# Optimization experiments

Measured on AMD Instinct MI355X. Metric: run time of the kernel, lower is better.

## Reference

```python
import jax, jax.numpy as jnp
import numpy as np

B, S, H, N, D = 2, 2048, 1024, 16, 64  # batch, seq, hidden, heads, head_dim


def setup_inputs() -> dict:
    key = jax.random.key(0)
    ks = jax.random.split(key, 7)
    sc = 0.02
    return {
        "query": jax.random.normal(ks[0], (B, S, H), jnp.float32),
        "key": jax.random.normal(ks[1], (B, S, H), jnp.float32),
        "value": jax.random.normal(ks[2], (B, S, H), jnp.float32),
        "Wq": jax.random.normal(ks[3], (N, H, D), jnp.float32) * sc,
        "Wk": jax.random.normal(ks[4], (N, H, D), jnp.float32) * sc,
        "Wv": jax.random.normal(ks[5], (N, H, D), jnp.float32) * sc,
        "Wo": jax.random.normal(ks[6], (H, H), jnp.float32) * sc,
    }


def reference(query, key, value, Wq, Wk, Wv, Wo):
    # Per-head projections (all heads batched): q,k,v -> [B, N, S, D]
    q = jnp.einsum('bsh,nhd->bnsd', query, Wq)
    k = jnp.einsum('bsh,nhd->bnsd', key, Wk)
    v = jnp.einsum('bsh,nhd->bnsd', value, Wv)
    scale = jnp.sqrt(jnp.asarray(D, q.dtype))
    # scaled dot-product attention, no mask, dropout=0 (eval mode)
    scores = jnp.einsum('bnqd,bnkd->bnqk', q, k) / scale  # [B, N, S, S]
    attn = jax.nn.softmax(scores, axis=-1)
    ctx = jnp.einsum('bnqk,bnkd->bnqd', attn, v)  # [B, N, S, D]
    # concat heads (head order matches the module's per-head list order)
    concat = ctx.transpose(0, 2, 1, 3).reshape(B, S, N * D)  # [B, S, H]
    out = concat @ Wo  # output projection, bias-free
    return out, attn
```

## Files before the change

kernel.cpp:

```cpp
#include <hip/hip_runtime.h>
#include <hip/hip_bf16.h>

using bf16 = __hip_bfloat16;
typedef __bf16 bf16x8 __attribute__((ext_vector_type(8)));
typedef float f32x4 __attribute__((ext_vector_type(4)));

__device__ __forceinline__ void async16(const void* g, void* l) {
    __builtin_amdgcn_global_load_lds((const __attribute__((address_space(1))) void*)g,
                                     (__attribute__((address_space(3))) void*)l, 16, 0, 0);
}
__device__ __forceinline__ bf16x8 ld8(const bf16* p) {
    return *reinterpret_cast<const bf16x8*>(p);
}
__device__ __forceinline__ unsigned short bfbits(float f) {
    bf16 h = __float2bfloat16(f);
    return *reinterpret_cast<unsigned short*>(&h);
}


__global__ __launch_bounds__(256) void cast_kernel(const float* __restrict__ q, const float* __restrict__ k,
                                                   const float* __restrict__ v, bf16* __restrict__ dst) {
    int z = blockIdx.z;
    const float* src = (z == 0) ? q : (z == 1) ? k : v;
    bf16* d = dst + (size_t)z * 4194304u;
    size_t i = ((size_t)blockIdx.x * 256 + threadIdx.x) * 4;
    float4 f = *(const float4*)(src + i);
    ushort4 pk = make_ushort4(bfbits(f.x), bfbits(f.y), bfbits(f.z), bfbits(f.w));
    *(ushort4*)(d + i) = pk;
}

__global__ __launch_bounds__(256) void wt_kernel(const float* __restrict__ wq, const float* __restrict__ wk,
                                                 const float* __restrict__ wv, bf16* __restrict__ wt) {
    int z = blockIdx.z;
    const float* W = (z == 0) ? wq : (z == 1) ? wk : wv;
    bf16* Wt = wt + (size_t)z * (1024u * 1024u);
    int n = blockIdx.y, h0 = blockIdx.x * 64;
    __shared__ float tile[64][65];
    int t = threadIdx.x, row = t >> 2, cq = t & 3;
#pragma unroll
    for (int u = 0; u < 4; u++) {
        int col = cq * 16 + u * 4;
        float4 f = *(const float4*)(W + (size_t)(n * 1024 + h0 + row) * 64 + col);
        tile[row][col] = f.x; tile[row][col + 1] = f.y; tile[row][col + 2] = f.z; tile[row][col + 3] = f.w;
    }
    __syncthreads();
#pragma unroll
    for (int u = 0; u < 4; u++) {
        int hl = cq * 16 + u * 4;
        ushort4 pk = make_ushort4(bfbits(tile[hl][row]), bfbits(tile[hl + 1][row]),
                                  bfbits(tile[hl + 2][row]), bfbits(tile[hl + 3][row]));
        *(ushort4*)(Wt + (size_t)(n * 64 + row) * 1024 + h0 + hl) = pk;
    }
}

__global__ __launch_bounds__(256) void wo_kernel(const float* __restrict__ Wo, bf16* __restrict__ Wot) {
    int h0 = blockIdx.x * 64, j0 = blockIdx.y * 64;
    __shared__ float tile[64][65];
    int t = threadIdx.x, row = t >> 2, cq = t & 3;
#pragma unroll
    for (int u = 0; u < 4; u++) {
        int col = cq * 16 + u * 4;
        float4 f = *(const float4*)(Wo + (size_t)(h0 + row) * 1024 + j0 + col);
        tile[row][col] = f.x; tile[row][col + 1] = f.y; tile[row][col + 2] = f.z; tile[row][col + 3] = f.w;
    }
    __syncthreads();
#pragma unroll
    for (int u = 0; u < 4; u++) {
        int hl = cq * 16 + u * 4;
        ushort4 pk = make_ushort4(bfbits(tile[hl][row]), bfbits(tile[hl + 1][row]),
                                  bfbits(tile[hl + 2][row]), bfbits(tile[hl + 3][row]));
        *(ushort4*)(Wot + (size_t)(j0 + row) * 1024 + h0 + hl) = pk;
    }
}

__global__ __launch_bounds__(256) void proj_kernel(const bf16* __restrict__ Xall, const bf16* __restrict__ Wall,
                                                   bf16* __restrict__ qb, bf16* __restrict__ kb,
                                                   bf16* __restrict__ vt) {
    int z = blockIdx.z;
    const bf16* X = Xall + (size_t)z * (4096u * 1024u);
    const bf16* W = Wall + (size_t)z * (1024u * 1024u);
    __shared__ bf16 sA[128 * 64];
    __shared__ bf16 sB[128 * 64];
    int t = threadIdx.x, lane = t & 63, q4 = lane >> 4, cl = lane & 15, w = t >> 6;
    int wm = (w >> 1) * 64, wn = (w & 1) * 64;
    int m0 = blockIdx.x * 128, n0 = blockIdx.y * 128;
    f32x4 acc[4][4] = {};
    for (int k0 = 0; k0 < 1024; k0 += 64) {
#pragma unroll
        for (int it = 0; it < 4; it++) {
            int j = it * 256 + t;
            int row = j >> 3, sl = j & 7, g = sl ^ (row & 7);
            async16(X + (size_t)(m0 + row) * 1024 + k0 + g * 8, sA + j * 8);
            async16(W + (size_t)(n0 + row) * 1024 + k0 + g * 8, sB + j * 8);
        }
        __syncthreads();
#pragma unroll
        for (int ks = 0; ks < 2; ks++) {
            bf16x8 af[4], bfr[4];
#pragma unroll
            for (int mi = 0; mi < 4; mi++) {
                int row = wm + mi * 16 + cl;
                af[mi] = ld8(sA + row * 64 + ((ks * 4 + q4) ^ (row & 7)) * 8);
            }
#pragma unroll
            for (int ni = 0; ni < 4; ni++) {
                int row = wn + ni * 16 + cl;
                bfr[ni] = ld8(sB + row * 64 + ((ks * 4 + q4) ^ (row & 7)) * 8);
            }
#pragma unroll
            for (int mi = 0; mi < 4; mi++)
#pragma unroll
                for (int ni = 0; ni < 4; ni++)
                    acc[mi][ni] = __builtin_amdgcn_mfma_f32_16x16x32_bf16(af[mi], bfr[ni], acc[mi][ni], 0, 0, 0);
        }
        __syncthreads();
    }
    if (z < 2) {
        bf16* dst = (z == 0) ? qb : kb;
#pragma unroll
        for (int mi = 0; mi < 4; mi++)
#pragma unroll
            for (int ni = 0; ni < 4; ni++) {
                int col = n0 + wn + ni * 16 + cl;
                int hn = col >> 6, dd = col & 63;
#pragma unroll
                for (int i = 0; i < 4; i++) {
                    int row = m0 + wm + mi * 16 + q4 * 4 + i;
                    int b = row >> 11, s = row & 2047;
                    dst[(size_t)((b * 16 + hn) * 2048 + s) * 64 + dd] = __float2bfloat16(acc[mi][ni][i]);
                }
            }
    } else {
#pragma unroll
        for (int mi = 0; mi < 4; mi++)
#pragma unroll
            for (int ni = 0; ni < 4; ni++) {
                int col = n0 + wn + ni * 16 + cl;
                int hn = col >> 6, dd = col & 63;
                int row0 = m0 + wm + mi * 16 + q4 * 4;
                int b = row0 >> 11, s = row0 & 2047;
                ushort4 pk = make_ushort4(bfbits(acc[mi][ni][0]), bfbits(acc[mi][ni][1]),
                                          bfbits(acc[mi][ni][2]), bfbits(acc[mi][ni][3]));
                *(ushort4*)(vt + (size_t)((b * 16 + hn) * 64 + dd) * 2048 + s) = pk;
            }
    }
}

__global__ __launch_bounds__(256) void attn_kernel(const bf16* __restrict__ qb, const bf16* __restrict__ kb,
                                                   const bf16* __restrict__ vt, bf16* __restrict__ cc,
                                                   float* __restrict__ attn) {
    __shared__ bf16 sQ[64 * 64];
    __shared__ bf16 sK[64 * 64];
    __shared__ bf16 sV[64 * 64];
    __shared__ bf16 sP[64 * 64];
    __shared__ float srow[64];
    __shared__ float sinv[64];
    int t = threadIdx.x, lane = t & 63, q4 = lane >> 4, cl = lane & 15, w = t >> 6;
    int bn = blockIdx.y;
    int s0 = blockIdx.x * 64;
    const bf16* qh = qb + (size_t)bn * 2048 * 64;
    const bf16* kh = kb + (size_t)bn * 2048 * 64;
    const bf16* vh = vt + (size_t)bn * 64 * 2048;
    float* ah = attn + (size_t)bn * 2048 * 2048;

    if (t < 64) srow[t] = 0.f;
#pragma unroll
    for (int it = 0; it < 2; it++) {
        int j = it * 256 + t;
        int row = j >> 3, sl = j & 7, g = sl ^ (row & 7);
        async16(qh + (size_t)(s0 + row) * 64 + g * 8, sQ + j * 8);
    }

    float rs[4][4] = {};
    for (int ch = 0; ch < 32; ch++) {
#pragma unroll
        for (int it = 0; it < 2; it++) {
            int j = it * 256 + t;
            int row = j >> 3, sl = j & 7, g = sl ^ (row & 7);
            async16(kh + (size_t)(ch * 64 + row) * 64 + g * 8, sK + j * 8);
        }
        __syncthreads();
        bf16x8 bk[2];
#pragma unroll
        for (int ks = 0; ks < 2; ks++) {
            int row = w * 16 + cl;
            bk[ks] = ld8(sK + row * 64 + ((ks * 4 + q4) ^ (row & 7)) * 8);
        }
#pragma unroll
        for (int mi = 0; mi < 4; mi++) {
            f32x4 sa = {0.f, 0.f, 0.f, 0.f};
#pragma unroll
            for (int ks = 0; ks < 2; ks++) {
                int row = mi * 16 + cl;
                bf16x8 aq = ld8(sQ + row * 64 + ((ks * 4 + q4) ^ (row & 7)) * 8);
                sa = __builtin_amdgcn_mfma_f32_16x16x32_bf16(aq, bk[ks], sa, 0, 0, 0);
            }
#pragma unroll
            for (int i = 0; i < 4; i++) rs[mi][i] += __expf(sa[i] * 0.125f);
        }
        __syncthreads();
    }
#pragma unroll
    for (int mi = 0; mi < 4; mi++)
#pragma unroll
        for (int i = 0; i < 4; i++) {
            float v = rs[mi][i];
            v += __shfl_xor(v, 1);
            v += __shfl_xor(v, 2);
            v += __shfl_xor(v, 4);
            v += __shfl_xor(v, 8);
            if (cl == 0) atomicAdd(&srow[mi * 16 + q4 * 4 + i], v);
        }
    __syncthreads();
    if (t < 64) sinv[t] = 1.0f / srow[t];
    __syncthreads();
    float invA[4][4];
#pragma unroll
    for (int mi = 0; mi < 4; mi++)
#pragma unroll
        for (int i = 0; i < 4; i++) invA[mi][i] = sinv[mi * 16 + q4 * 4 + i];
    float invC[4];
#pragma unroll
    for (int i = 0; i < 4; i++) invC[i] = sinv[w * 16 + q4 * 4 + i];

    f32x4 ctx[4] = {};
    for (int ch = 0; ch < 32; ch++) {
#pragma unroll
        for (int it = 0; it < 2; it++) {
            int j = it * 256 + t;
            int row = j >> 3, sl = j & 7, g = sl ^ (row & 7);
            async16(kh + (size_t)(ch * 64 + row) * 64 + g * 8, sK + j * 8);
            async16(vh + (size_t)row * 2048 + ch * 64 + g * 8, sV + j * 8);
        }
        __syncthreads();
        bf16x8 bk[2];
#pragma unroll
        for (int ks = 0; ks < 2; ks++) {
            int row = w * 16 + cl;
            bk[ks] = ld8(sK + row * 64 + ((ks * 4 + q4) ^ (row & 7)) * 8);
        }
#pragma unroll
        for (int mi = 0; mi < 4; mi++) {
            f32x4 sa = {0.f, 0.f, 0.f, 0.f};
#pragma unroll
            for (int ks = 0; ks < 2; ks++) {
                int row = mi * 16 + cl;
                bf16x8 aq = ld8(sQ + row * 64 + ((ks * 4 + q4) ^ (row & 7)) * 8);
                sa = __builtin_amdgcn_mfma_f32_16x16x32_bf16(aq, bk[ks], sa, 0, 0, 0);
            }
            int coll = ch * 64 + w * 16 + cl;
#pragma unroll
            for (int i = 0; i < 4; i++) {
                float p = __expf(sa[i] * 0.125f);
                int r = mi * 16 + q4 * 4 + i;
                __builtin_nontemporal_store(p * invA[mi][i], ah + (size_t)(s0 + r) * 2048 + coll);
                int c2 = w * 16 + cl;
                sP[r * 64 + ((c2 >> 3) ^ (r & 7)) * 8 + (c2 & 7)] = __float2bfloat16(p);
            }
        }
        __syncthreads();
#pragma unroll
        for (int ks = 0; ks < 2; ks++) {
            int rp = w * 16 + cl;
            bf16x8 ap = ld8(sP + rp * 64 + ((ks * 4 + q4) ^ (rp & 7)) * 8);
#pragma unroll
            for (int ni = 0; ni < 4; ni++) {
                int rv = ni * 16 + cl;
                bf16x8 bv = ld8(sV + rv * 64 + ((ks * 4 + q4) ^ (rv & 7)) * 8);
                ctx[ni] = __builtin_amdgcn_mfma_f32_16x16x32_bf16(ap, bv, ctx[ni], 0, 0, 0);
            }
        }
        __syncthreads();
    }
    int b = bn >> 4, n = bn & 15;
#pragma unroll
    for (int ni = 0; ni < 4; ni++)
#pragma unroll
        for (int i = 0; i < 4; i++) {
            int sg = s0 + w * 16 + q4 * 4 + i;
            int dd = ni * 16 + cl;
            cc[(size_t)(b * 2048 + sg) * 1024 + n * 64 + dd] = __float2bfloat16(ctx[ni][i] * invC[i]);
        }
}

__global__ __launch_bounds__(256) void out_kernel(const bf16* __restrict__ A, const bf16* __restrict__ W,
                                                  float* __restrict__ out) {
    __shared__ bf16 sA[128 * 64];
    __shared__ bf16 sB[128 * 64];
    int t = threadIdx.x, lane = t & 63, q4 = lane >> 4, cl = lane & 15, w = t >> 6;
    int wm = (w >> 1) * 64, wn = (w & 1) * 64;
    int m0 = blockIdx.x * 128, n0 = blockIdx.y * 128;
    f32x4 acc[4][4] = {};
    for (int k0 = 0; k0 < 1024; k0 += 64) {
#pragma unroll
        for (int it = 0; it < 4; it++) {
            int j = it * 256 + t;
            int row = j >> 3, sl = j & 7, g = sl ^ (row & 7);
            async16(A + (size_t)(m0 + row) * 1024 + k0 + g * 8, sA + j * 8);
            async16(W + (size_t)(n0 + row) * 1024 + k0 + g * 8, sB + j * 8);
        }
        __syncthreads();
#pragma unroll
        for (int ks = 0; ks < 2; ks++) {
            bf16x8 af[4], bfr[4];
#pragma unroll
            for (int mi = 0; mi < 4; mi++) {
                int row = wm + mi * 16 + cl;
                af[mi] = ld8(sA + row * 64 + ((ks * 4 + q4) ^ (row & 7)) * 8);
            }
#pragma unroll
            for (int ni = 0; ni < 4; ni++) {
                int row = wn + ni * 16 + cl;
                bfr[ni] = ld8(sB + row * 64 + ((ks * 4 + q4) ^ (row & 7)) * 8);
            }
#pragma unroll
            for (int mi = 0; mi < 4; mi++)
#pragma unroll
                for (int ni = 0; ni < 4; ni++)
                    acc[mi][ni] = __builtin_amdgcn_mfma_f32_16x16x32_bf16(af[mi], bfr[ni], acc[mi][ni], 0, 0, 0);
        }
        __syncthreads();
    }
#pragma unroll
    for (int mi = 0; mi < 4; mi++)
#pragma unroll
        for (int ni = 0; ni < 4; ni++) {
            int col = n0 + wn + ni * 16 + cl;
#pragma unroll
            for (int i = 0; i < 4; i++) {
                int row = m0 + wm + mi * 16 + q4 * 4 + i;
                out[(size_t)row * 1024 + col] = acc[mi][ni][i];
            }
        }
}

extern "C" void kernel_launch(void* const* d_in, const int* in_sizes, int n_in,
                              void* d_out, int out_size, void* d_ws, size_t ws_size,
                              hipStream_t stream) {
    const float* query = (const float*)d_in[0];
    const float* key = (const float*)d_in[1];
    const float* value = (const float*)d_in[2];
    const float* Wq = (const float*)d_in[3];
    const float* Wk = (const float*)d_in[4];
    const float* Wv = (const float*)d_in[5];
    const float* Wo = (const float*)d_in[6];
    float* out = (float*)d_out;
    float* attn = out + 4194304;

    char* w = (char*)d_ws;
    bf16* Xbf = (bf16*)(w);
    bf16* ccb = (bf16*)(w);
    bf16* Wt = (bf16*)(w + (24u << 20));
    bf16* Wot = (bf16*)(w + (30u << 20));
    bf16* qbuf = (bf16*)(w + (32u << 20));
    bf16* kbuf = (bf16*)(w + (40u << 20));
    bf16* vtb = (bf16*)(w + (48u << 20));

    cast_kernel<<<dim3(4096, 1, 3), 256, 0, stream>>>(query, key, value, Xbf);
    wt_kernel<<<dim3(16, 16, 3), 256, 0, stream>>>(Wq, Wk, Wv, Wt);
    wo_kernel<<<dim3(16, 16), 256, 0, stream>>>(Wo, Wot);
    proj_kernel<<<dim3(32, 8, 3), 256, 0, stream>>>(Xbf, Wt, qbuf, kbuf, vtb);
    attn_kernel<<<dim3(32, 32), 256, 0, stream>>>(qbuf, kbuf, vtb, ccb, attn);
    out_kernel<<<dim3(32, 8), 256, 0, stream>>>(ccb, Wot, out);
}
```

Before: 757.9 us.

## Double-buffer K/V loads in attention, keep Q in registers, vectorize attn stores

Folds the softmax scale and log2(e) into Q at projection time so exp2f can be used directly. The attention kernel now keeps Q fragments in registers, reuses the Q LDS buffer for P, and double-buffers K and V so the next chunk's global-to-LDS copies overlap compute, using manual waitcnt and barriers. The attention matrix is written as 16-byte vector nontemporal stores read back from the bf16 P tile, instead of scalar stores. The grid axes are also swapped so blocks of the same head run together. Risks include the manual vmcnt counts being wrong, and attn precision dropping because the normalized probabilities are now taken from bf16 P.

```diff
diff --git a/kernel.cpp b/kernel.cpp
--- a/kernel.cpp
+++ b/kernel.cpp
@@ -3,6 +3,7 @@
 
 using bf16 = __hip_bfloat16;
 typedef __bf16 bf16x8 __attribute__((ext_vector_type(8)));
+typedef __bf16 bf16x4 __attribute__((ext_vector_type(4)));
 typedef float f32x4 __attribute__((ext_vector_type(4)));
 
 __device__ __forceinline__ void async16(const void* g, void* l) {
@@ -117,6 +118,7 @@
     }
     if (z < 2) {
         bf16* dst = (z == 0) ? qb : kb;
+        float qs = (z == 0) ? 0.18033688011112042f : 1.0f;
 #pragma unroll
         for (int mi = 0; mi < 4; mi++)
 #pragma unroll
@@ -127,7 +129,7 @@
                 for (int i = 0; i < 4; i++) {
                     int row = m0 + wm + mi * 16 + q4 * 4 + i;
                     int b = row >> 11, s = row & 2047;
-                    dst[(size_t)((b * 16 + hn) * 2048 + s) * 64 + dd] = __float2bfloat16(acc[mi][ni][i]);
+                    dst[(size_t)((b * 16 + hn) * 2048 + s) * 64 + dd] = __float2bfloat16(acc[mi][ni][i] * qs);
                 }
             }
     } else {
@@ -149,15 +151,14 @@
 __global__ __launch_bounds__(256) void attn_kernel(const bf16* __restrict__ qb, const bf16* __restrict__ kb,
                                                    const bf16* __restrict__ vt, bf16* __restrict__ cc,
                                                    float* __restrict__ attn) {
-    __shared__ bf16 sQ[64 * 64];
-    __shared__ bf16 sK[64 * 64];
-    __shared__ bf16 sV[64 * 64];
-    __shared__ bf16 sP[64 * 64];
+    __shared__ bf16 sQP[64 * 64];
+    __shared__ bf16 sKb[64 * 64];
+    __shared__ bf16 sVb[2][64 * 64];
     __shared__ float srow[64];
     __shared__ float sinv[64];
     int t = threadIdx.x, lane = t & 63, q4 = lane >> 4, cl = lane & 15, w = t >> 6;
-    int bn = blockIdx.y;
-    int s0 = blockIdx.x * 64;
+    int bn = blockIdx.x;
+    int s0 = blockIdx.y * 64;
     const bf16* qh = qb + (size_t)bn * 2048 * 64;
     const bf16* kh = kb + (size_t)bn * 2048 * 64;
     const bf16* vh = vt + (size_t)bn * 64 * 2048;
@@ -168,35 +169,45 @@
     for (int it = 0; it < 2; it++) {
         int j = it * 256 + t;
         int row = j >> 3, sl = j & 7, g = sl ^ (row & 7);
-        async16(qh + (size_t)(s0 + row) * 64 + g * 8, sQ + j * 8);
-    }
+        async16(qh + (size_t)(s0 + row) * 64 + g * 8, sQP + j * 8);
+        async16(kh + (size_t)row * 64 + g * 8, sKb + j * 8);
+    }
+    __syncthreads();
+
+    bf16x8 aq[4][2];
+#pragma unroll
+    for (int mi = 0; mi < 4; mi++)
+#pragma unroll
+        for (int ks = 0; ks < 2; ks++) {
+            int row = mi * 16 + cl;
+            aq[mi][ks] = ld8(sQP + row * 64 + ((ks * 4 + q4) ^ (row & 7)) * 8);
+        }
 
     float rs[4][4] = {};
     for (int ch = 0; ch < 32; ch++) {
-#pragma unroll
-        for (int it = 0; it < 2; it++) {
-            int j = it * 256 + t;
-            int row = j >> 3, sl = j & 7, g = sl ^ (row & 7);
-            async16(kh + (size_t)(ch * 64 + row) * 64 + g * 8, sK + j * 8);
-        }
-        __syncthreads();
+        const bf16* kcur = (ch & 1) ? sVb[0] : sKb;
+        bf16* knxt = (ch & 1) ? sKb : sVb[0];
+        if (ch < 31) {
+#pragma unroll
+            for (int it = 0; it < 2; it++) {
+                int j = it * 256 + t;
+                int row = j >> 3, sl = j & 7, g = sl ^ (row & 7);
+                async16(kh + (size_t)((ch + 1) * 64 + row) * 64 + g * 8, knxt + j * 8);
+            }
+        }
         bf16x8 bk[2];
 #pragma unroll
         for (int ks = 0; ks < 2; ks++) {
             int row = w * 16 + cl;
-            bk[ks] = ld8(sK + row * 64 + ((ks * 4 + q4) ^ (row & 7)) * 8);
+            bk[ks] = ld8(kcur + row * 64 + ((ks * 4 + q4) ^ (row & 7)) * 8);
         }
 #pragma unroll
         for (int mi = 0; mi < 4; mi++) {
             f32x4 sa = {0.f, 0.f, 0.f, 0.f};
-#pragma unroll
-            for (int ks = 0; ks < 2; ks++) {
-                int row = mi * 16 + cl;
-                bf16x8 aq = ld8(sQ + row * 64 + ((ks * 4 + q4) ^ (row & 7)) * 8);
-                sa = __builtin_amdgcn_mfma_f32_16x16x32_bf16(aq, bk[ks], sa, 0, 0, 0);
-            }
-#pragma unroll
-            for (int i = 0; i < 4; i++) rs[mi][i] += __expf(sa[i] * 0.125f);
+            sa = __builtin_amdgcn_mfma_f32_16x16x32_bf16(aq[mi][0], bk[0], sa, 0, 0, 0);
+            sa = __builtin_amdgcn_mfma_f32_16x16x32_bf16(aq[mi][1], bk[1], sa, 0, 0, 0);
+#pragma unroll
+            for (int i = 0; i < 4; i++) rs[mi][i] += exp2f(sa[i]);
         }
         __syncthreads();
     }
@@ -214,63 +225,86 @@
     __syncthreads();
     if (t < 64) sinv[t] = 1.0f / srow[t];
     __syncthreads();
-    float invA[4][4];
-#pragma unroll
-    for (int mi = 0; mi < 4; mi++)
-#pragma unroll
-        for (int i = 0; i < 4; i++) invA[mi][i] = sinv[mi * 16 + q4 * 4 + i];
     float invC[4];
 #pragma unroll
     for (int i = 0; i < 4; i++) invC[i] = sinv[w * 16 + q4 * 4 + i];
+
+#pragma unroll
+    for (int it = 0; it < 2; it++) {
+        int j = it * 256 + t;
+        int row = j >> 3, sl = j & 7, g = sl ^ (row & 7);
+        async16(kh + (size_t)row * 64 + g * 8, sKb + j * 8);
+        async16(vh + (size_t)row * 2048 + g * 8, sVb[0] + j * 8);
+    }
+    __syncthreads();
 
     f32x4 ctx[4] = {};
     for (int ch = 0; ch < 32; ch++) {
-#pragma unroll
-        for (int it = 0; it < 2; it++) {
-            int j = it * 256 + t;
-            int row = j >> 3, sl = j & 7, g = sl ^ (row & 7);
-            async16(kh + (size_t)(ch * 64 + row) * 64 + g * 8, sK + j * 8);
-            async16(vh + (size_t)row * 2048 + ch * 64 + g * 8, sV + j * 8);
-        }
-        __syncthreads();
+        int cur = ch & 1;
+        if (ch < 31) {
+#pragma unroll
+            for (int it = 0; it < 2; it++) {
+                int j = it * 256 + t;
+                int row = j >> 3, sl = j & 7, g = sl ^ (row & 7);
+                async16(vh + (size_t)row * 2048 + (ch + 1) * 64 + g * 8, sVb[cur ^ 1] + j * 8);
+            }
+        }
+        __builtin_amdgcn_sched_barrier(0);
         bf16x8 bk[2];
 #pragma unroll
         for (int ks = 0; ks < 2; ks++) {
             int row = w * 16 + cl;
-            bk[ks] = ld8(sK + row * 64 + ((ks * 4 + q4) ^ (row & 7)) * 8);
-        }
+            bk[ks] = ld8(sKb + row * 64 + ((ks * 4 + q4) ^ (row & 7)) * 8);
+        }
+        int c2 = w * 16 + cl;
 #pragma unroll
         for (int mi = 0; mi < 4; mi++) {
             f32x4 sa = {0.f, 0.f, 0.f, 0.f};
-#pragma unroll
-            for (int ks = 0; ks < 2; ks++) {
-                int row = mi * 16 + cl;
-                bf16x8 aq = ld8(sQ + row * 64 + ((ks * 4 + q4) ^ (row & 7)) * 8);
-                sa = __builtin_amdgcn_mfma_f32_16x16x32_bf16(aq, bk[ks], sa, 0, 0, 0);
-            }
-            int coll = ch * 64 + w * 16 + cl;
+            sa = __builtin_amdgcn_mfma_f32_16x16x32_bf16(aq[mi][0], bk[0], sa, 0, 0, 0);
+            sa = __builtin_amdgcn_mfma_f32_16x16x32_bf16(aq[mi][1], bk[1], sa, 0, 0, 0);
 #pragma unroll
             for (int i = 0; i < 4; i++) {
-                float p = __expf(sa[i] * 0.125f);
+                float p = exp2f(sa[i]);
                 int r = mi * 16 + q4 * 4 + i;
-                __builtin_nontemporal_store(p * invA[mi][i], ah + (size_t)(s0 + r) * 2048 + coll);
-                int c2 = w * 16 + cl;
-                sP[r * 64 + ((c2 >> 3) ^ (r & 7)) * 8 + (c2 & 7)] = __float2bfloat16(p);
-            }
-        }
-        __syncthreads();
+                sQP[r * 64 + ((c2 >> 3) ^ (r & 7)) * 8 + (c2 & 7)] = __float2bfloat16(p);
+            }
+        }
+        asm volatile("s_waitcnt lgkmcnt(0)" ::: "memory");
+        __builtin_amdgcn_sched_barrier(0);
+        __builtin_amdgcn_s_barrier();
+        if (ch < 31) {
+#pragma unroll
+            for (int it = 0; it < 2; it++) {
+                int j = it * 256 + t;
+                int row = j >> 3, sl = j & 7, g = sl ^ (row & 7);
+                async16(kh + (size_t)((ch + 1) * 64 + row) * 64 + g * 8, sKb + j * 8);
+            }
+        }
+        __builtin_amdgcn_sched_barrier(0);
+        const bf16* vcur = sVb[cur];
 #pragma unroll
         for (int ks = 0; ks < 2; ks++) {
             int rp = w * 16 + cl;
-            bf16x8 ap = ld8(sP + rp * 64 + ((ks * 4 + q4) ^ (rp & 7)) * 8);
+            bf16x8 ap = ld8(sQP + rp * 64 + ((ks * 4 + q4) ^ (rp & 7)) * 8);
 #pragma unroll
             for (int ni = 0; ni < 4; ni++) {
                 int rv = ni * 16 + cl;
-                bf16x8 bv = ld8(sV + rv * 64 + ((ks * 4 + q4) ^ (rv & 7)) * 8);
+                bf16x8 bv = ld8(vcur + rv * 64 + ((ks * 4 + q4) ^ (rv & 7)) * 8);
                 ctx[ni] = __builtin_amdgcn_mfma_f32_16x16x32_bf16(ap, bv, ctx[ni], 0, 0, 0);
             }
         }
-        __syncthreads();
+#pragma unroll
+        for (int it = 0; it < 4; it++) {
+            int j = it * 256 + t;
+            int row = j >> 4, qc = j & 15;
+            bf16x4 p4 = *reinterpret_cast<const bf16x4*>(sQP + row * 64 + ((qc >> 1) ^ (row & 7)) * 8 + (qc & 1) * 4);
+            float inv = sinv[row];
+            f32x4 o = {(float)p4[0] * inv, (float)p4[1] * inv, (float)p4[2] * inv, (float)p4[3] * inv};
+            __builtin_nontemporal_store(o, reinterpret_cast<f32x4*>(ah + (size_t)(s0 + row) * 2048 + ch * 64 + qc * 4));
+        }
+        asm volatile("s_waitcnt vmcnt(4) lgkmcnt(0)" ::: "memory");
+        __builtin_amdgcn_sched_barrier(0);
+        __builtin_amdgcn_s_barrier();
     }
     int b = bn >> 4, n = bn & 15;
 #pragma unroll
```

After: 760.4 us. About the same (+0.3%).
